# Performance work log

Hardware: AMD Instinct MI355X
Metric: run time of the kernel (lower is better)

## Reference

```python
import jax, jax.numpy as jnp
import numpy as np

N, E = 50000, 800000
IN, H1, H2, HEADS, EMB = 128, 32, 32, 4, 128
NEG_SLOPE = 0.2  # DGL GATConv default leaky_relu slope


def setup_inputs() -> dict:
    key = jax.random.key(0)
    ks = jax.random.split(key, 14)
    s = 0.05
    return {
        "x": jax.random.normal(ks[0], (N, IN), jnp.float32),
        "src": jax.random.randint(ks[1], (E,), 0, N, jnp.int32),
        "dst": jax.random.randint(ks[2], (E,), 0, N, jnp.int32),
        "W1": jax.random.normal(ks[3], (IN, HEADS * H1), jnp.float32) * s,
        "al1": jax.random.normal(ks[4], (HEADS, H1), jnp.float32) * s,
        "ar1": jax.random.normal(ks[5], (HEADS, H1), jnp.float32) * s,
        "b1": jnp.zeros((HEADS * H1,), jnp.float32),
        "W2": jax.random.normal(ks[6], (HEADS * H1, HEADS * H2), jnp.float32) * s,
        "al2": jax.random.normal(ks[7], (HEADS, H2), jnp.float32) * s,
        "ar2": jax.random.normal(ks[8], (HEADS, H2), jnp.float32) * s,
        "b2": jnp.zeros((HEADS * H2,), jnp.float32),
        "Wp": jax.random.normal(ks[9], (HEADS * H2, EMB), jnp.float32) * s,
        "bp": jnp.zeros((EMB,), jnp.float32),
    }


def gat_layer(x, W, al, ar, b, src, dst, heads, d_out):
    n = x.shape[0]
    feat = (x @ W).reshape(n, heads, d_out)            # [N,H,D]
    el = (feat * al).sum(-1)                           # [N,H]
    er = (feat * ar).sum(-1)                           # [N,H]
    e = jax.nn.leaky_relu(el[src] + er[dst], NEG_SLOPE)  # [E,H]
    # edge softmax over destination segments
    m = jax.ops.segment_max(e, dst, num_segments=n)    # [N,H] (-inf for empty)
    ex = jnp.exp(e - m[dst])                           # [E,H]
    z = jax.ops.segment_sum(ex, dst, num_segments=n)   # [N,H]
    alpha = ex / z[dst]                                # [E,H]
    msg = alpha[:, :, None] * feat[src]                # [E,H,D]
    out = jax.ops.segment_sum(msg, dst, num_segments=n)  # [N,H,D]
    return out + b.reshape(1, heads, d_out)


def reference(x, src, dst, W1, al1, ar1, b1, W2, al2, ar2, b2, Wp, bp):
    h = gat_layer(x, W1, al1, ar1, b1, src, dst, HEADS, H1).reshape(N, -1)
    h = gat_layer(h, W2, al2, ar2, b2, src, dst, HEADS, H2).reshape(N, -1)
    out = h @ Wp + bp
    return (h, out)
```

## Files before the change

kernel.cpp:

```cpp
#include <hip/hip_runtime.h>
#include <hip/hip_bf16.h>

#define N_NODES 50000
#define HEADS 4
#define DHEAD 32
#define F 128
#define NEG_SLOPE 0.2f

typedef unsigned int uint;
typedef unsigned short ushort;
typedef __attribute__((ext_vector_type(8))) short bf16x8;
typedef __attribute__((ext_vector_type(4))) float f32x4;

__device__ __forceinline__ float bf2f(ushort u) {
    union { uint i; float f; } c; c.i = ((uint)u) << 16; return c.f;
}
__device__ __forceinline__ ushort f2bf(float f) {
    union { float f; uint i; } c; c.f = f;
    uint u = c.i + 0x7FFF + ((c.i >> 16) & 1);
    return (ushort)(u >> 16);
}
__device__ __forceinline__ float sel4(int h, float a, float b, float c, float d) {
    return (h & 2) ? ((h & 1) ? d : c) : ((h & 1) ? b : a);
}

__global__ void rank_hist_kernel(const int* __restrict__ dst, int* __restrict__ counts,
                                 int* __restrict__ rank, int E) {
    int i = blockIdx.x * 256 + threadIdx.x;
    if (i < E) rank[i] = atomicAdd(&counts[dst[i]], 1);
}

__global__ __launch_bounds__(256) void scanA_kernel(const int* __restrict__ counts,
                                                    int* __restrict__ local_sc,
                                                    int* __restrict__ partials,
                                                    int* __restrict__ blockbin,
                                                    int N, int NB) {
    __shared__ int lbin[64];
    int tid = threadIdx.x;
    if (tid < 64) lbin[tid] = 0;
    __syncthreads();
    int i = blockIdx.x * 256 + tid;
    int v = (i < N) ? counts[i] : 0;
    if (i < N) atomicAdd(&lbin[v < 63 ? v : 63], 1);
    int lane = tid & 63;
    int w = tid >> 6;
    int x = v;
#pragma unroll
    for (int off = 1; off < 64; off <<= 1) {
        int t = __shfl_up(x, off);
        if (lane >= off) x += t;
    }
    __shared__ int wsum[4];
    if (lane == 63) wsum[w] = x;
    __syncthreads();
    int wpre = 0;
#pragma unroll
    for (int k = 0; k < 4; k++)
        if (k < w) wpre += wsum[k];
    if (i < N) local_sc[i] = x - v + wpre;
    if (tid == 255) partials[blockIdx.x] = wpre + x;
    __syncthreads();
    if (tid < 64) blockbin[tid * NB + blockIdx.x] = lbin[tid];
}

__global__ __launch_bounds__(256) void scanB_kernel(int* __restrict__ partials, int NP,
                                                    int* __restrict__ blockbin, int M) {
    int tid = threadIdx.x;
    int lane = tid & 63;
    int w = tid >> 6;
    __shared__ int wsum[4];
    {
        int v = (tid < NP) ? partials[tid] : 0;
        int x = v;
#pragma unroll
        for (int off = 1; off < 64; off <<= 1) {
            int t = __shfl_up(x, off);
            if (lane >= off) x += t;
        }
        if (lane == 63) wsum[w] = x;
        __syncthreads();
        int wpre = 0;
#pragma unroll
        for (int k = 0; k < 4; k++)
            if (k < w) wpre += wsum[k];
        if (tid < NP) partials[tid] = x - v + wpre;
        __syncthreads();
    }
    {
        int chunk = (M + 255) / 256;
        int lo = tid * chunk;
        int hi = lo + chunk; if (hi > M) hi = M; if (lo > M) lo = M;
        int sum = 0;
        for (int i = lo; i < hi; i++) sum += blockbin[i];
        int x = sum;
#pragma unroll
        for (int off = 1; off < 64; off <<= 1) {
            int t = __shfl_up(x, off);
            if (lane >= off) x += t;
        }
        if (lane == 63) wsum[w] = x;
        __syncthreads();
        int wpre = 0;
#pragma unroll
        for (int k = 0; k < 4; k++)
            if (k < w) wpre += wsum[k];
        int pre = x - sum + wpre;
        for (int i = lo; i < hi; i++) {
            int c = blockbin[i];
            blockbin[i] = pre;
            pre += c;
        }
    }
}

__global__ __launch_bounds__(256) void scanC_kernel(int* __restrict__ offs,
                                                    const int* __restrict__ partials,
                                                    const int* __restrict__ counts,
                                                    const int* __restrict__ blockbin,
                                                    int* __restrict__ perm,
                                                    int N, int E, int NB) {
    __shared__ int lcur[64];
    int tid = threadIdx.x;
    if (tid < 64) lcur[tid] = blockbin[tid * NB + blockIdx.x];
    __syncthreads();
    int i = blockIdx.x * 256 + tid;
    if (i < N) {
        offs[i] += partials[blockIdx.x];
        int d = counts[i];
        int pos = atomicAdd(&lcur[d < 63 ? d : 63], 1);
        perm[pos] = i;
    }
    if (i == 0) offs[N] = E;
}

__global__ void posfix_kernel(const int* __restrict__ dst, const int* __restrict__ offs,
                              int* __restrict__ rank, int E) {
    int i = blockIdx.x * 256 + threadIdx.x;
    if (i < E) rank[i] += offs[dst[i]];
}

#define SCH 2048
__global__ __launch_bounds__(256) void scatter_ranged_kernel(
    const int* __restrict__ src, const int* __restrict__ pos,
    int* __restrict__ csr_src, int E) {
    int range = blockIdx.x & 7;
    int chunk = blockIdx.x >> 3;
    int base = chunk * SCH + threadIdx.x;
    int lo = (int)(((long long)range * E) >> 3);
    int hi = (int)(((long long)(range + 1) * E) >> 3);
#pragma unroll
    for (int k = 0; k < SCH / 256; k++) {
        int i = base + k * 256;
        if (i < E) {
            int p = pos[i];
            if (p >= lo && p < hi) csr_src[p] = src[i];
        }
    }
}

__global__ __launch_bounds__(256) void wtrans_kernel(
    const float* __restrict__ W1, const float* __restrict__ W2,
    const float* __restrict__ Wp,
    const float* __restrict__ al1, const float* __restrict__ ar1,
    const float* __restrict__ al2, const float* __restrict__ ar2,
    ushort* __restrict__ WT) {
    if (blockIdx.x < 3) {
        const float* W = (blockIdx.x == 0) ? W1 : (blockIdx.x == 1) ? W2 : Wp;
        ushort* T = WT + (size_t)blockIdx.x * 128 * 128;
        for (int i = threadIdx.x; i < 128 * 128; i += 256) {
            int r = i >> 7, c = i & 127;
            T[c * 128 + r] = f2bf(W[i]);
        }
    } else {
        const float* W   = (blockIdx.x == 3) ? W1 : W2;
        const float* a_l = (blockIdx.x == 3) ? al1 : al2;
        const float* a_r = (blockIdx.x == 3) ? ar1 : ar2;
        ushort* T = WT + 3 * 128 * 128 + (blockIdx.x - 3) * 16 * 128;
        for (int i = threadIdx.x; i < 16 * 128; i += 256) {
            int c = i >> 7, k = i & 127;
            float v = 0.f;
            if (c < 8) {
                int h = c & 3;
                const float* a  = (c < 4) ? (a_l + h * 32) : (a_r + h * 32);
                const float* wr = W + k * 128 + h * 32;
#pragma unroll
                for (int d = 0; d < 32; d++) v += wr[d] * a[d];
            }
            T[i] = f2bf(v);
        }
    }
}

template <bool A_FP32, bool OUT_BF16, bool BIAS, bool ELER>
__global__ __launch_bounds__(256) void mfma_gemm_kernel(
    const void* __restrict__ Av, const ushort* __restrict__ BT,
    const float* __restrict__ bias, const ushort* __restrict__ ALR,
    void* __restrict__ Cv, float* __restrict__ el, float* __restrict__ er, int M) {
    int wid = threadIdx.x >> 6;
    int lane = threadIdx.x & 63;
    int row0 = blockIdx.x * 64 + wid * 16;
    int rsub = lane & 15;
    int kg = lane >> 4;
    int row = row0 + rsub;
    int rowc = (row < M) ? row : (M - 1);

    bf16x8 af[4];
    if (A_FP32) {
        const float* A = (const float*)Av;
        const float* ap = A + (size_t)rowc * 128 + kg * 8;
#pragma unroll
        for (int ks = 0; ks < 4; ks++) {
            float4 lo = *(const float4*)(ap + ks * 32);
            float4 hi = *(const float4*)(ap + ks * 32 + 4);
            bf16x8 v;
            v[0] = (short)f2bf(lo.x); v[1] = (short)f2bf(lo.y);
            v[2] = (short)f2bf(lo.z); v[3] = (short)f2bf(lo.w);
            v[4] = (short)f2bf(hi.x); v[5] = (short)f2bf(hi.y);
            v[6] = (short)f2bf(hi.z); v[7] = (short)f2bf(hi.w);
            af[ks] = v;
        }
    } else {
        const ushort* A = (const ushort*)Av;
        const ushort* ap = A + (size_t)rowc * 128 + kg * 8;
#pragma unroll
        for (int ks = 0; ks < 4; ks++) af[ks] = *(const bf16x8*)(ap + ks * 32);
    }

    f32x4 acc[8];
#pragma unroll
    for (int ct = 0; ct < 8; ct++) acc[ct] = (f32x4){0.f, 0.f, 0.f, 0.f};

    const ushort* bp = BT + (size_t)rsub * 128 + kg * 8;
#pragma unroll
    for (int ks = 0; ks < 4; ks++) {
#pragma unroll
        for (int ct = 0; ct < 8; ct++) {
            bf16x8 bf = *(const bf16x8*)(bp + (size_t)ct * 16 * 128 + ks * 32);
            acc[ct] = __builtin_amdgcn_mfma_f32_16x16x32_bf16(af[ks], bf, acc[ct], 0, 0, 0);
        }
    }

    f32x4 acce = (f32x4){0.f, 0.f, 0.f, 0.f};
    if (ELER) {
        const ushort* ep = ALR + rsub * 128 + kg * 8;
#pragma unroll
        for (int ks = 0; ks < 4; ks++) {
            bf16x8 eb = *(const bf16x8*)(ep + ks * 32);
            acce = __builtin_amdgcn_mfma_f32_16x16x32_bf16(af[ks], eb, acce, 0, 0, 0);
        }
    }

    if (row0 >= M) return;

#pragma unroll
    for (int ct = 0; ct < 8; ct++) {
        int col = ct * 16 + rsub;
        float bv = BIAS ? bias[col] : 0.f;
#pragma unroll
        for (int r = 0; r < 4; r++) {
            int gr = row0 + kg * 4 + r;
            if (gr < M) {
                float v = acc[ct][r] + bv;
                if (OUT_BF16) ((ushort*)Cv)[(size_t)gr * 128 + col] = f2bf(v);
                else          ((float*)Cv)[(size_t)gr * 128 + col] = v;
            }
        }
    }

    if (ELER && rsub < 8) {
#pragma unroll
        for (int r = 0; r < 4; r++) {
            int gr = row0 + kg * 4 + r;
            if (gr < M) {
                if (rsub < 4) el[(size_t)gr * 4 + rsub] = acce[r];
                else          er[(size_t)gr * 4 + (rsub - 4)] = acce[r];
            }
        }
    }
}

template <bool F32OUT>
__global__ __launch_bounds__(256) void aggregate_kernel(
    const ushort* __restrict__ featb, const float* __restrict__ el,
    const float* __restrict__ er, const float* __restrict__ bias,
    const int* __restrict__ offsets, const int* __restrict__ csr_src,
    const int* __restrict__ perm, void* __restrict__ outv, int N) {
    int tid = threadIdx.x;
    int gl = tid & 15;
    int lane = tid & 63;
    int slot = blockIdx.x * 16 + (tid >> 4);
    if (slot >= N) return;
    int n = perm[slot];
    int start = offsets[n], end = offsets[n + 1];

    float4 erv = *(const float4*)(er + (size_t)n * 4);
    float er_h[4] = {erv.x, erv.y, erv.z, erv.w};

    float m[4], s[4];
#pragma unroll
    for (int h = 0; h < 4; h++) { m[h] = -1e30f; s[h] = 0.f; }

    for (int e = start + gl; e < end; e += 16) {
        int sv = csr_src[e];
        float4 ev = *(const float4*)(el + (size_t)sv * 4);
        float elh[4] = {ev.x, ev.y, ev.z, ev.w};
#pragma unroll
        for (int h = 0; h < 4; h++) {
            float v = elh[h] + er_h[h];
            v = (v >= 0.f) ? v : NEG_SLOPE * v;
            float mn = fmaxf(m[h], v);
            s[h] = s[h] * __expf(m[h] - mn) + __expf(v - mn);
            m[h] = mn;
        }
    }
#pragma unroll
    for (int off = 1; off < 16; off <<= 1) {
#pragma unroll
        for (int h = 0; h < 4; h++) {
            float mo = __shfl_xor(m[h], off);
            float so = __shfl_xor(s[h], off);
            float mn = fmaxf(m[h], mo);
            s[h] = s[h] * __expf(m[h] - mn) + so * __expf(mo - mn);
            m[h] = mn;
        }
    }

    int h0 = gl >> 2;
    int j  = gl & 3;
    int c0 = gl * 8;
    float mh  = sel4(h0, m[0], m[1], m[2], m[3]);
    float sh  = sel4(h0, s[0], s[1], s[2], s[3]);
    float erh = sel4(h0, er_h[0], er_h[1], er_h[2], er_h[3]);
    float rzh = (end > start) ? 1.0f / sh : 0.f;
    int bidx = lane & 60;

    float acc[8] = {};
    for (int e = start; e < end; e += 4) {
        int rem = end - e;
        int ej = e + ((j < rem) ? j : 0);
        int svj = csr_src[ej];
        float v = el[(size_t)svj * 4 + h0] + erh;
        v = (v >= 0.f) ? v : NEG_SLOPE * v;
        float a = __expf(v - mh) * rzh;
        if (j >= rem) a = 0.f;
#pragma unroll
        for (int jj = 0; jj < 4; jj++) {
            float ajj = __shfl(a, bidx | jj);
            int svjj  = __shfl(svj, bidx | jj);
            uint4 f0 = *(const uint4*)(featb + (size_t)svjj * 128 + c0);
            acc[0] = fmaf(ajj, bf2f(f0.x & 0xFFFF), acc[0]);
            acc[1] = fmaf(ajj, bf2f(f0.x >> 16),    acc[1]);
            acc[2] = fmaf(ajj, bf2f(f0.y & 0xFFFF), acc[2]);
            acc[3] = fmaf(ajj, bf2f(f0.y >> 16),    acc[3]);
            acc[4] = fmaf(ajj, bf2f(f0.z & 0xFFFF), acc[4]);
            acc[5] = fmaf(ajj, bf2f(f0.z >> 16),    acc[5]);
            acc[6] = fmaf(ajj, bf2f(f0.w & 0xFFFF), acc[6]);
            acc[7] = fmaf(ajj, bf2f(f0.w >> 16),    acc[7]);
        }
    }

    float4 b0 = *(const float4*)(bias + c0);
    float4 b1 = *(const float4*)(bias + c0 + 4);
    float o[8];
    o[0] = acc[0] + b0.x; o[1] = acc[1] + b0.y; o[2] = acc[2] + b0.z; o[3] = acc[3] + b0.w;
    o[4] = acc[4] + b1.x; o[5] = acc[5] + b1.y; o[6] = acc[6] + b1.z; o[7] = acc[7] + b1.w;
    if (F32OUT) {
        float* outf = (float*)outv;
        float4 w0, w1;
        w0.x = o[0]; w0.y = o[1]; w0.z = o[2]; w0.w = o[3];
        w1.x = o[4]; w1.y = o[5]; w1.z = o[6]; w1.w = o[7];
        *(float4*)(outf + (size_t)n * 128 + c0) = w0;
        *(float4*)(outf + (size_t)n * 128 + c0 + 4) = w1;
    } else {
        ushort* outb = (ushort*)outv;
        uint4 p;
        p.x = (uint)f2bf(o[0]) | ((uint)f2bf(o[1]) << 16);
        p.y = (uint)f2bf(o[2]) | ((uint)f2bf(o[3]) << 16);
        p.z = (uint)f2bf(o[4]) | ((uint)f2bf(o[5]) << 16);
        p.w = (uint)f2bf(o[6]) | ((uint)f2bf(o[7]) << 16);
        *(uint4*)(outb + (size_t)n * 128 + c0) = p;
    }
}

extern "C" void kernel_launch(void* const* d_in, const int* in_sizes, int n_in,
                              void* d_out, int out_size, void* d_ws, size_t ws_size,
                              hipStream_t stream) {
    const float* x   = (const float*)d_in[0];
    const int*   src = (const int*)d_in[1];
    const int*   dst = (const int*)d_in[2];
    const float* W1  = (const float*)d_in[3];
    const float* al1 = (const float*)d_in[4];
    const float* ar1 = (const float*)d_in[5];
    const float* b1  = (const float*)d_in[6];
    const float* W2  = (const float*)d_in[7];
    const float* al2 = (const float*)d_in[8];
    const float* ar2 = (const float*)d_in[9];
    const float* b2  = (const float*)d_in[10];
    const float* Wp  = (const float*)d_in[11];
    const float* bp  = (const float*)d_in[12];

    const int N = in_sizes[0] / F;
    const int E = in_sizes[1];

    float* h_out = (float*)d_out;
    float* p_out = h_out + (size_t)N * F;

    const int NB = (N + 255) / 256;
    const int EB = (E + 255) / 256;

    char* w = (char*)d_ws;
    ushort* featb   = (ushort*)w;
    ushort* h1b     = featb + (size_t)N * F;
    float* el       = (float*)(h1b + (size_t)N * F);
    float* er       = el + (size_t)N * 4;
    int*   offs     = (int*)(er + (size_t)N * 4);
    int*   counts   = offs + (N + 1);
    int*   perm     = counts + N;
    int*   blockbin = perm + N;
    int*   rank     = blockbin + 64 * NB;
    int*   csrsrc   = rank + E;
    int*   partials = csrsrc + E;
    ushort* WT      = (ushort*)(partials + 256);

    hipMemsetAsync(counts, 0, (size_t)N * 4, stream);
    rank_hist_kernel<<<EB, 256, 0, stream>>>(dst, counts, rank, E);
    scanA_kernel<<<NB, 256, 0, stream>>>(counts, offs, partials, blockbin, N, NB);
    scanB_kernel<<<1, 256, 0, stream>>>(partials, NB, blockbin, 64 * NB);
    scanC_kernel<<<NB, 256, 0, stream>>>(offs, partials, counts, blockbin, perm, N, E, NB);
    posfix_kernel<<<EB, 256, 0, stream>>>(dst, offs, rank, E);
    scatter_ranged_kernel<<<8 * ((E + SCH - 1) / SCH), 256, 0, stream>>>(src, rank, csrsrc, E);

    wtrans_kernel<<<5, 256, 0, stream>>>(W1, W2, Wp, al1, ar1, al2, ar2, WT);
    ushort* WT1  = WT;
    ushort* WT2  = WT + 128 * 128;
    ushort* WTp  = WT + 2 * 128 * 128;
    ushort* ALR1 = WT + 3 * 128 * 128;
    ushort* ALR2 = ALR1 + 16 * 128;

    int ggrid = (N + 63) / 64;
    int agrid = (N + 15) / 16;

    mfma_gemm_kernel<true, true, false, true><<<ggrid, 256, 0, stream>>>(
        x, WT1, nullptr, ALR1, featb, el, er, N);
    aggregate_kernel<false><<<agrid, 256, 0, stream>>>(
        featb, el, er, b1, offs, csrsrc, perm, h1b, N);

    mfma_gemm_kernel<false, true, false, true><<<ggrid, 256, 0, stream>>>(
        h1b, WT2, nullptr, ALR2, featb, el, er, N);
    aggregate_kernel<true><<<agrid, 256, 0, stream>>>(
        featb, el, er, b2, offs, csrsrc, perm, h_out, N);

    mfma_gemm_kernel<true, false, true, false><<<ggrid, 256, 0, stream>>>(
        h_out, WTp, bp, nullptr, p_out, nullptr, nullptr, N);
}
```

Measured before the change: 262.2 us.

## Split GAT aggregation across heads with one block per head

The aggregation kernel now launches four times as many blocks, each handling a single attention head for 16 destination nodes. Each 16-lane group computes the softmax statistics for one head only, and each lane gathers 2 bf16 columns per edge instead of 8, processing 16 edges per chunk. This raises parallelism and cuts per-thread softmax work. In exchange, each thread issues narrower gathers, and csr_src/el reads plus the softmax reduction are repeated once per head, adding redundant memory traffic.

```diff
diff --git a/kernel.cpp b/kernel.cpp
--- a/kernel.cpp
+++ b/kernel.cpp
@@ -19,9 +19,6 @@
     union { float f; uint i; } c; c.f = f;
     uint u = c.i + 0x7FFF + ((c.i >> 16) & 1);
     return (ushort)(u >> 16);
-}
-__device__ __forceinline__ float sel4(int h, float a, float b, float c, float d) {
-    return (h & 2) ? ((h & 1) ? d : c) : ((h & 1) ? b : a);
 }
 
 __global__ void rank_hist_kernel(const int* __restrict__ dst, int* __restrict__ counts,
@@ -280,105 +277,83 @@
 }
 
 template <bool F32OUT>
-__global__ __launch_bounds__(256) void aggregate_kernel(
+__global__ __launch_bounds__(256) void aggregate_head_kernel(
     const ushort* __restrict__ featb, const float* __restrict__ el,
     const float* __restrict__ er, const float* __restrict__ bias,
     const int* __restrict__ offsets, const int* __restrict__ csr_src,
     const int* __restrict__ perm, void* __restrict__ outv, int N) {
     int tid = threadIdx.x;
     int gl = tid & 15;
-    int lane = tid & 63;
-    int slot = blockIdx.x * 16 + (tid >> 4);
+    int h = blockIdx.x & 3;
+    int slot = (blockIdx.x >> 2) * 16 + (tid >> 4);
     if (slot >= N) return;
     int n = perm[slot];
     int start = offsets[n], end = offsets[n + 1];
-
-    float4 erv = *(const float4*)(er + (size_t)n * 4);
-    float er_h[4] = {erv.x, erv.y, erv.z, erv.w};
-
-    float m[4], s[4];
-#pragma unroll
-    for (int h = 0; h < 4; h++) { m[h] = -1e30f; s[h] = 0.f; }
-
+    float erh = er[(size_t)n * 4 + h];
+
+    float m = -1e30f, s = 0.f;
     for (int e = start + gl; e < end; e += 16) {
         int sv = csr_src[e];
-        float4 ev = *(const float4*)(el + (size_t)sv * 4);
-        float elh[4] = {ev.x, ev.y, ev.z, ev.w};
-#pragma unroll
-        for (int h = 0; h < 4; h++) {
-            float v = elh[h] + er_h[h];
-            v = (v >= 0.f) ? v : NEG_SLOPE * v;
-            float mn = fmaxf(m[h], v);
-            s[h] = s[h] * __expf(m[h] - mn) + __expf(v - mn);
-            m[h] = mn;
-        }
+        float v = el[(size_t)sv * 4 + h] + erh;
+        v = (v >= 0.f) ? v : NEG_SLOPE * v;
+        float mn = fmaxf(m, v);
+        s = s * __expf(m - mn) + __expf(v - mn);
+        m = mn;
     }
 #pragma unroll
     for (int off = 1; off < 16; off <<= 1) {
-#pragma unroll
-        for (int h = 0; h < 4; h++) {
-            float mo = __shfl_xor(m[h], off);
-            float so = __shfl_xor(s[h], off);
-            float mn = fmaxf(m[h], mo);
-            s[h] = s[h] * __expf(m[h] - mn) + so * __expf(mo - mn);
-            m[h] = mn;
-        }
-    }
-
-    int h0 = gl >> 2;
-    int j  = gl & 3;
-    int c0 = gl * 8;
-    float mh  = sel4(h0, m[0], m[1], m[2], m[3]);
-    float sh  = sel4(h0, s[0], s[1], s[2], s[3]);
-    float erh = sel4(h0, er_h[0], er_h[1], er_h[2], er_h[3]);
-    float rzh = (end > start) ? 1.0f / sh : 0.f;
-    int bidx = lane & 60;
-
-    float acc[8] = {};
-    for (int e = start; e < end; e += 4) {
-        int rem = end - e;
-        int ej = e + ((j < rem) ? j : 0);
+        float mo = __shfl_xor(m, off);
+        float so = __shfl_xor(s, off);
+        float mn = fmaxf(m, mo);
+        s = s * __expf(m - mn) + so * __expf(mo - mn);
+        m = mn;
+    }
+    float rz = (end > start) ? 1.0f / s : 0.f;
+
+    int c0 = h * 32 + gl * 2;
+    int gbase = (tid & 63) & 48;
+    float acc0 = 0.f, acc1 = 0.f;
+
+    int eb = start;
+    for (; eb + 16 <= end; eb += 16) {
+        int svj = csr_src[eb + gl];
+        float v = el[(size_t)svj * 4 + h] + erh;
+        v = (v >= 0.f) ? v : NEG_SLOPE * v;
+        float a = __expf(v - m) * rz;
+#pragma unroll
+        for (int jj = 0; jj < 16; jj++) {
+            float ajj = __shfl(a, gbase | jj);
+            int svjj  = __shfl(svj, gbase | jj);
+            uint f = *(const uint*)(featb + (size_t)svjj * 128 + c0);
+            acc0 = fmaf(ajj, bf2f(f & 0xFFFF), acc0);
+            acc1 = fmaf(ajj, bf2f(f >> 16), acc1);
+        }
+    }
+    int rem = end - eb;
+    if (rem > 0) {
+        int ej = eb + ((gl < rem) ? gl : 0);
         int svj = csr_src[ej];
-        float v = el[(size_t)svj * 4 + h0] + erh;
+        float v = el[(size_t)svj * 4 + h] + erh;
         v = (v >= 0.f) ? v : NEG_SLOPE * v;
-        float a = __expf(v - mh) * rzh;
-        if (j >= rem) a = 0.f;
-#pragma unroll
-        for (int jj = 0; jj < 4; jj++) {
-            float ajj = __shfl(a, bidx | jj);
-            int svjj  = __shfl(svj, bidx | jj);
-            uint4 f0 = *(const uint4*)(featb + (size_t)svjj * 128 + c0);
-            acc[0] = fmaf(ajj, bf2f(f0.x & 0xFFFF), acc[0]);
-            acc[1] = fmaf(ajj, bf2f(f0.x >> 16),    acc[1]);
-            acc[2] = fmaf(ajj, bf2f(f0.y & 0xFFFF), acc[2]);
-            acc[3] = fmaf(ajj, bf2f(f0.y >> 16),    acc[3]);
-            acc[4] = fmaf(ajj, bf2f(f0.z & 0xFFFF), acc[4]);
-            acc[5] = fmaf(ajj, bf2f(f0.z >> 16),    acc[5]);
-            acc[6] = fmaf(ajj, bf2f(f0.w & 0xFFFF), acc[6]);
-            acc[7] = fmaf(ajj, bf2f(f0.w >> 16),    acc[7]);
-        }
-    }
-
-    float4 b0 = *(const float4*)(bias + c0);
-    float4 b1 = *(const float4*)(bias + c0 + 4);
-    float o[8];
-    o[0] = acc[0] + b0.x; o[1] = acc[1] + b0.y; o[2] = acc[2] + b0.z; o[3] = acc[3] + b0.w;
-    o[4] = acc[4] + b1.x; o[5] = acc[5] + b1.y; o[6] = acc[6] + b1.z; o[7] = acc[7] + b1.w;
+        float a = __expf(v - m) * rz;
+        if (gl >= rem) a = 0.f;
+        for (int jj = 0; jj < rem; jj++) {
+            float ajj = __shfl(a, gbase | jj);
+            int svjj  = __shfl(svj, gbase | jj);
+            uint f = *(const uint*)(featb + (size_t)svjj * 128 + c0);
+            acc0 = fmaf(ajj, bf2f(f & 0xFFFF), acc0);
+            acc1 = fmaf(ajj, bf2f(f >> 16), acc1);
+        }
+    }
+
+    float o0 = acc0 + bias[c0];
+    float o1 = acc1 + bias[c0 + 1];
     if (F32OUT) {
-        float* outf = (float*)outv;
-        float4 w0, w1;
-        w0.x = o[0]; w0.y = o[1]; w0.z = o[2]; w0.w = o[3];
-        w1.x = o[4]; w1.y = o[5]; w1.z = o[6]; w1.w = o[7];
-        *(float4*)(outf + (size_t)n * 128 + c0) = w0;
-        *(float4*)(outf + (size_t)n * 128 + c0 + 4) = w1;
+        float2 w; w.x = o0; w.y = o1;
+        *(float2*)((float*)outv + (size_t)n * 128 + c0) = w;
     } else {
-        ushort* outb = (ushort*)outv;
-        uint4 p;
-        p.x = (uint)f2bf(o[0]) | ((uint)f2bf(o[1]) << 16);
-        p.y = (uint)f2bf(o[2]) | ((uint)f2bf(o[3]) << 16);
-        p.z = (uint)f2bf(o[4]) | ((uint)f2bf(o[5]) << 16);
-        p.w = (uint)f2bf(o[6]) | ((uint)f2bf(o[7]) << 16);
-        *(uint4*)(outb + (size_t)n * 128 + c0) = p;
+        uint p = (uint)f2bf(o0) | ((uint)f2bf(o1) << 16);
+        *(uint*)((ushort*)outv + (size_t)n * 128 + c0) = p;
     }
 }
 
@@ -438,16 +413,16 @@
     ushort* ALR2 = ALR1 + 16 * 128;
 
     int ggrid = (N + 63) / 64;
-    int agrid = (N + 15) / 16;
+    int agrid = 4 * ((N + 15) / 16);
 
     mfma_gemm_kernel<true, true, false, true><<<ggrid, 256, 0, stream>>>(
         x, WT1, nullptr, ALR1, featb, el, er, N);
-    aggregate_kernel<false><<<agrid, 256, 0, stream>>>(
+    aggregate_head_kernel<false><<<agrid, 256, 0, stream>>>(
         featb, el, er, b1, offs, csrsrc, perm, h1b, N);
 
     mfma_gemm_kernel<false, true, false, true><<<ggrid, 256, 0, stream>>>(
         h1b, WT2, nullptr, ALR2, featb, el, er, N);
-    aggregate_kernel<true><<<agrid, 256, 0, stream>>>(
+    aggregate_head_kernel<true><<<agrid, 256, 0, stream>>>(
         featb, el, er, b2, offs, csrsrc, perm, h_out, N);
 
     mfma_gemm_kernel<true, false, true, false><<<ggrid, 256, 0, stream>>>(
```

Measured after the change: 335.2 us. 1.28x slower.
